# Kernel tuning notes

Hardware: AMD Instinct MI355X
Metric: run time of the kernel (lower is better)

Reference implementation:

```python
import jax, jax.numpy as jnp
import numpy as np

N_HEADS = 16
D_MODEL = 1024
D_K = D_MODEL // N_HEADS


def setup_inputs() -> dict:
    key = jax.random.key(0)
    ks = jax.random.split(key, 9)
    B, L = 4, 2048
    s = 1.0 / np.sqrt(D_MODEL)
    x = jax.random.normal(ks[0], (B, L, D_MODEL), dtype=jnp.float32)
    mask = jnp.tril(jnp.ones((L, L), dtype=jnp.int32))  # causal [L, L]
    Wq = jax.random.normal(ks[1], (D_MODEL, D_MODEL), dtype=jnp.float32) * s
    Wk = jax.random.normal(ks[2], (D_MODEL, D_MODEL), dtype=jnp.float32) * s
    Wv = jax.random.normal(ks[3], (D_MODEL, D_MODEL), dtype=jnp.float32) * s
    Wo = jax.random.normal(ks[4], (D_MODEL, D_MODEL), dtype=jnp.float32) * s
    bq = jnp.zeros((D_MODEL,), jnp.float32)
    bk = jnp.zeros((D_MODEL,), jnp.float32)
    bv = jnp.zeros((D_MODEL,), jnp.float32)
    bo = jnp.zeros((D_MODEL,), jnp.float32)
    return {"x": x, "mask": mask, "Wq": Wq, "bq": bq, "Wk": Wk, "bk": bk,
            "Wv": Wv, "bv": bv, "Wo": Wo, "bo": bo}


def reference(x, mask, Wq, bq, Wk, bk, Wv, bv, Wo, bo):
    B, L, _ = x.shape
    # projections -> [B, H, L, d_k]
    def split_heads(t):
        return t.reshape(B, L, N_HEADS, D_K).transpose(0, 2, 1, 3)
    Q = split_heads(x @ Wq + bq)
    K = split_heads(x @ Wk + bk)
    V = split_heads(x @ Wv + bv)
    orig_dtype = Q.dtype
    # fp32 upcast for scores (faithful to source)
    scores = jnp.einsum('bhqd,bhkd->bhqk', Q.astype(jnp.float32),
                        K.astype(jnp.float32)) / np.sqrt(D_K)
    # orig dtype is float32 -> masked fill with -inf
    scores = jnp.where(mask == 0, -jnp.inf, scores).astype(orig_dtype)
    attn = jax.nn.softmax(scores, axis=-1)  # dropout p=0 -> identity (eval)
    out = jnp.einsum('bhqk,bhkd->bhqd', attn, V)
    out = out.transpose(0, 2, 1, 3).reshape(B, L, D_MODEL)
    return out @ Wo + bo
```

## Files before the change

kernel.cpp:

```cpp
#include <hip/hip_runtime.h>

#define DMODEL 1024
#define NTOK   8192
#define SEQ    2048
#define NH     16
#define DK     64

typedef short short8  __attribute__((ext_vector_type(8)));
typedef short short4v __attribute__((ext_vector_type(4)));
typedef float floatx4 __attribute__((ext_vector_type(4)));

__device__ __forceinline__ unsigned short f2bf(float f) {
  unsigned int u = __float_as_uint(f);
  u += 0x7fffu + ((u >> 16) & 1u);
  return (unsigned short)(u >> 16);
}

__device__ __forceinline__ void async16(short* lds, const short* g) {
  __builtin_amdgcn_global_load_lds(
      (const __attribute__((address_space(1))) void*)g,
      (__attribute__((address_space(3))) void*)lds, 16, 0, 0);
}

__global__ void prep_kernel(const float* __restrict__ x, ushort4* __restrict__ xb,
                            const float* __restrict__ W0, const float* __restrict__ W1,
                            const float* __restrict__ W2, const float* __restrict__ W3,
                            short* __restrict__ T0, short* __restrict__ T1,
                            short* __restrict__ T2, short* __restrict__ T3) {
  const int z = blockIdx.z;
  const int tx = threadIdx.x, ty = threadIdx.y;
  if (z == 4) {
    const float4* xv = (const float4*)x;
    int i = (blockIdx.y * 32 + blockIdx.x) * 256 + ty * 32 + tx;
#pragma unroll
    for (int u = 0; u < 8; ++u) {
      int idx = i + u * 262144;
      float4 v = xv[idx];
      ushort4 o;
      o.x = f2bf(v.x); o.y = f2bf(v.y); o.z = f2bf(v.z); o.w = f2bf(v.w);
      xb[idx] = o;
    }
    return;
  }
  __shared__ float tile[32][33];
  const float* W = (z == 0) ? W0 : (z == 1) ? W1 : (z == 2) ? W2 : W3;
  short*      Wt = (z == 0) ? T0 : (z == 1) ? T1 : (z == 2) ? T2 : T3;
  int bx = blockIdx.x, by = blockIdx.y;
#pragma unroll
  for (int j = 0; j < 4; ++j)
    tile[ty + j * 8][tx] = W[(size_t)(by * 32 + ty + j * 8) * DMODEL + bx * 32 + tx];
  __syncthreads();
#pragma unroll
  for (int j = 0; j < 4; ++j)
    Wt[(size_t)(bx * 32 + ty + j * 8) * DMODEL + by * 32 + tx] =
        (short)f2bf(tile[tx][ty + j * 8]);
}

__global__ __launch_bounds__(256, 2) void gemm_qkv_fused(
    const short* __restrict__ xb,
    const short* __restrict__ Wqt, const short* __restrict__ Wkt, const short* __restrict__ Wvt,
    const float* __restrict__ bq,  const float* __restrict__ bk,  const float* __restrict__ bv,
    short* __restrict__ Qb, short* __restrict__ Kb, short* __restrict__ Vt) {
  __shared__ __align__(16) short As[128 * 64];
  __shared__ __align__(16) short Bs[3][128 * 64];
  const int tid = threadIdx.x, lane = tid & 63, w = tid >> 6;
  const int wm = w >> 1, wn = w & 1, ln = lane & 15, quad = lane >> 4;
  const int m0 = blockIdx.y * 128, n0 = blockIdx.x * 128;

  floatx4 acc[3][4][4];
#pragma unroll
  for (int z = 0; z < 3; ++z)
#pragma unroll
    for (int i = 0; i < 4; ++i)
#pragma unroll
      for (int j = 0; j < 4; ++j) acc[z][i][j] = (floatx4){0.f, 0.f, 0.f, 0.f};

  const int lr8 = lane >> 3, fch = ((lane & 7) ^ lr8) * 8;
  const short* ga  = xb  + (size_t)(m0 + lr8) * DMODEL + fch;
  const short* gb0 = Wqt + (size_t)(n0 + lr8) * DMODEL + fch;
  const short* gb1 = Wkt + (size_t)(n0 + lr8) * DMODEL + fch;
  const short* gb2 = Wvt + (size_t)(n0 + lr8) * DMODEL + fch;

  for (int kb = 0; kb < DMODEL; kb += 64) {
    __syncthreads();
#pragma unroll
    for (int i = 0; i < 4; ++i) {
      const int rb = w * 32 + i * 8;
      const size_t go = (size_t)rb * DMODEL + kb;
      async16(As + rb * 64,        ga  + go);
      async16((short*)Bs[0] + rb * 64, gb0 + go);
      async16((short*)Bs[1] + rb * 64, gb1 + go);
      async16((short*)Bs[2] + rb * 64, gb2 + go);
    }
    __syncthreads();
#pragma unroll
    for (int kk = 0; kk < 2; ++kk) {
      short8 af[4];
#pragma unroll
      for (int t = 0; t < 4; ++t) {
        int row = wm * 64 + t * 16 + ln;
        af[t] = *(const short8*)(As + row * 64 + ((kk * 4 + quad) ^ (row & 7)) * 8);
      }
#pragma unroll
      for (int z = 0; z < 3; ++z) {
        short8 bf[4];
#pragma unroll
        for (int t = 0; t < 4; ++t) {
          int row = wn * 64 + t * 16 + ln;
          bf[t] = *(const short8*)(Bs[z] + row * 64 + ((kk * 4 + quad) ^ (row & 7)) * 8);
        }
#pragma unroll
        for (int mt = 0; mt < 4; ++mt)
#pragma unroll
          for (int nt = 0; nt < 4; ++nt)
            acc[z][mt][nt] = __builtin_amdgcn_mfma_f32_16x16x32_bf16(af[mt], bf[nt], acc[z][mt][nt], 0, 0, 0);
      }
    }
  }

#pragma unroll
  for (int z = 0; z < 2; ++z) {
    const float* bias = z ? bk : bq;
    short* out        = z ? Kb : Qb;
    const float scale = z ? 1.0f : 0.18033688011112042f;
#pragma unroll
    for (int mt = 0; mt < 4; ++mt)
#pragma unroll
      for (int nt = 0; nt < 4; ++nt) {
        int n = n0 + wn * 64 + nt * 16 + ln;
        float bb = bias[n];
        int h = n >> 6, d = n & 63;
#pragma unroll
        for (int r = 0; r < 4; ++r) {
          int m = m0 + wm * 64 + mt * 16 + quad * 4 + r;
          int b = m >> 11, l = m & 2047;
          out[(size_t)(b * NH + h) * (SEQ * DK) + (size_t)l * DK + d] =
              (short)f2bf((acc[z][mt][nt][r] + bb) * scale);
        }
      }
  }
#pragma unroll
  for (int mt = 0; mt < 4; ++mt)
#pragma unroll
    for (int nt = 0; nt < 4; ++nt) {
      int n = n0 + wn * 64 + nt * 16 + ln;
      float bb = bv[n];
      int h = n >> 6, d = n & 63;
      int mb = m0 + wm * 64 + mt * 16 + quad * 4;
      int b = mb >> 11, l = mb & 2047;
      short4v pk;
#pragma unroll
      for (int r = 0; r < 4; ++r) pk[r] = (short)f2bf(acc[2][mt][nt][r] + bb);
      *(short4v*)(Vt + ((size_t)(b * NH + h) * DK + d) * SEQ + l) = pk;
    }
}

__global__ __launch_bounds__(256) void gemm_out(
    const short* __restrict__ Ob, const short* __restrict__ Wot,
    const float* __restrict__ bo, float* __restrict__ outp) {
  __shared__ __align__(16) short As[128 * 64];
  __shared__ __align__(16) short Bs[128 * 64];
  const int tid = threadIdx.x, lane = tid & 63, w = tid >> 6;
  const int wm = w >> 1, wn = w & 1, ln = lane & 15, quad = lane >> 4;
  const int m0 = blockIdx.y * 128, n0 = blockIdx.x * 128;
  floatx4 acc[4][4];
#pragma unroll
  for (int i = 0; i < 4; ++i)
#pragma unroll
    for (int j = 0; j < 4; ++j) acc[i][j] = (floatx4){0.f, 0.f, 0.f, 0.f};
  const int lr8 = lane >> 3, fch = ((lane & 7) ^ lr8) * 8;
  const short* ga = Ob  + (size_t)(m0 + lr8) * DMODEL + fch;
  const short* gb = Wot + (size_t)(n0 + lr8) * DMODEL + fch;
  for (int kb = 0; kb < DMODEL; kb += 64) {
    __syncthreads();
#pragma unroll
    for (int i = 0; i < 4; ++i) {
      const int rb = w * 32 + i * 8;
      const size_t go = (size_t)rb * DMODEL + kb;
      async16(As + rb * 64, ga + go);
      async16(Bs + rb * 64, gb + go);
    }
    __syncthreads();
#pragma unroll
    for (int kk = 0; kk < 2; ++kk) {
      short8 af[4], bf[4];
#pragma unroll
      for (int t = 0; t < 4; ++t) {
        int ra = wm * 64 + t * 16 + ln, rb2 = wn * 64 + t * 16 + ln;
        af[t] = *(const short8*)(As + ra * 64 + ((kk * 4 + quad) ^ (ra & 7)) * 8);
        bf[t] = *(const short8*)(Bs + rb2 * 64 + ((kk * 4 + quad) ^ (rb2 & 7)) * 8);
      }
#pragma unroll
      for (int mt = 0; mt < 4; ++mt)
#pragma unroll
        for (int nt = 0; nt < 4; ++nt)
          acc[mt][nt] = __builtin_amdgcn_mfma_f32_16x16x32_bf16(af[mt], bf[nt], acc[mt][nt], 0, 0, 0);
    }
  }
#pragma unroll
  for (int mt = 0; mt < 4; ++mt)
#pragma unroll
    for (int nt = 0; nt < 4; ++nt) {
      int n = n0 + wn * 64 + nt * 16 + ln;
      float bb = bo[n];
#pragma unroll
      for (int r = 0; r < 4; ++r) {
        int m = m0 + wm * 64 + mt * 16 + quad * 4 + r;
        outp[(size_t)m * DMODEL + n] = acc[mt][nt][r] + bb;
      }
    }
}

#define FMAX 12.0f

template <bool DOL>
__device__ __forceinline__ void attn_step(
    const short* __restrict__ Ks, const short* __restrict__ Vs,
    short* __restrict__ Ps0, short* __restrict__ Ps1,
    const short8 qfL[2], const short8 qfH[2],
    floatx4 accL[4], floatx4 accH[4], float& lstL, float& lstH,
    int qrowL, int qrowH, int kt, int qiL, int qiH,
    int ln, int quad, int w) {
  floatx4 sL[4], sH[4];
#pragma unroll
  for (int i = 0; i < 4; ++i) {
    if (DOL) sL[i] = (floatx4){0.f, 0.f, 0.f, 0.f};
    sH[i] = (floatx4){0.f, 0.f, 0.f, 0.f};
  }
#pragma unroll
  for (int kk = 0; kk < 2; ++kk)
#pragma unroll
    for (int t = 0; t < 4; ++t) {
      short8 kf = *(const short8*)(Ks + (t * 16 + ln) * 64 + ((kk * 4 + quad) ^ (ln & 7)) * 8);
      if (DOL) sL[t] = __builtin_amdgcn_mfma_f32_16x16x32_bf16(kf, qfL[kk], sL[t], 0, 0, 0);
      sH[t] = __builtin_amdgcn_mfma_f32_16x16x32_bf16(kf, qfH[kk], sH[t], 0, 0, 0);
    }
  if (DOL && kt == qiL) {
#pragma unroll
    for (int t = 0; t < 4; ++t)
#pragma unroll
      for (int r = 0; r < 4; ++r)
        if (kt * 64 + t * 16 + quad * 4 + r > qrowL) sL[t][r] = -1.0e30f;
  }
  if (kt == qiH) {
#pragma unroll
    for (int t = 0; t < 4; ++t)
#pragma unroll
      for (int r = 0; r < 4; ++r)
        if (kt * 64 + t * 16 + quad * 4 + r > qrowH) sH[t][r] = -1.0e30f;
  }
  if (DOL) {
    float rs = 0.f;
#pragma unroll
    for (int t = 0; t < 4; ++t) {
      float p0 = __builtin_amdgcn_exp2f(sL[t][0] - FMAX);
      float p1 = __builtin_amdgcn_exp2f(sL[t][1] - FMAX);
      float p2 = __builtin_amdgcn_exp2f(sL[t][2] - FMAX);
      float p3 = __builtin_amdgcn_exp2f(sL[t][3] - FMAX);
      rs += (p0 + p1) + (p2 + p3);
      uint2 pk;
      pk.x = __builtin_amdgcn_perm(__float_as_uint(p1), __float_as_uint(p0), 0x07060302u);
      pk.y = __builtin_amdgcn_perm(__float_as_uint(p3), __float_as_uint(p2), 0x07060302u);
      *(uint2*)(Ps0 + (w * 16 + ln) * 72 + t * 16 + quad * 4) = pk;
    }
    lstL += rs;
  }
  {
    float rs = 0.f;
#pragma unroll
    for (int t = 0; t < 4; ++t) {
      float p0 = __builtin_amdgcn_exp2f(sH[t][0] - FMAX);
      float p1 = __builtin_amdgcn_exp2f(sH[t][1] - FMAX);
      float p2 = __builtin_amdgcn_exp2f(sH[t][2] - FMAX);
      float p3 = __builtin_amdgcn_exp2f(sH[t][3] - FMAX);
      rs += (p0 + p1) + (p2 + p3);
      uint2 pk;
      pk.x = __builtin_amdgcn_perm(__float_as_uint(p1), __float_as_uint(p0), 0x07060302u);
      pk.y = __builtin_amdgcn_perm(__float_as_uint(p3), __float_as_uint(p2), 0x07060302u);
      *(uint2*)(Ps1 + (w * 16 + ln) * 72 + t * 16 + quad * 4) = pk;
    }
    lstH += rs;
  }
  __threadfence_block();
#pragma unroll
  for (int kk = 0; kk < 2; ++kk) {
    short8 pfL, pfH;
    if (DOL) pfL = *(const short8*)(Ps0 + (w * 16 + ln) * 72 + kk * 32 + quad * 8);
    pfH = *(const short8*)(Ps1 + (w * 16 + ln) * 72 + kk * 32 + quad * 8);
#pragma unroll
    for (int dt = 0; dt < 4; ++dt) {
      short8 vf = *(const short8*)(Vs + (dt * 16 + ln) * 64 + ((kk * 4 + quad) ^ (ln & 7)) * 8);
      if (DOL) accL[dt] = __builtin_amdgcn_mfma_f32_16x16x32_bf16(vf, pfL, accL[dt], 0, 0, 0);
      accH[dt] = __builtin_amdgcn_mfma_f32_16x16x32_bf16(vf, pfH, accH[dt], 0, 0, 0);
    }
  }
}

__global__ __launch_bounds__(256, 4) void attn_kernel(
    const short* __restrict__ Qb, const short* __restrict__ Kb,
    const short* __restrict__ Vt, short* __restrict__ Ob) {
  __shared__ __align__(16) short Ks[64 * 64];
  __shared__ __align__(16) short Vs[64 * 64];
  __shared__ __align__(16) short Ps[2][64 * 72];
  const int tid = threadIdx.x, lane = tid & 63, w = tid >> 6;
  const int ln = lane & 15, quad = lane >> 4;
  const int pr = blockIdx.x;
  const int bh = blockIdx.y;
  const int qiL = pr, qiH = 31 - pr;
  const short* Qh = Qb + (size_t)bh * (SEQ * DK);
  const short* Kh = Kb + (size_t)bh * (SEQ * DK);
  const short* Vh = Vt + (size_t)bh * (DK * SEQ);

  const int qrowL = qiL * 64 + w * 16 + ln;
  const int qrowH = qiH * 64 + w * 16 + ln;
  short8 qfL[2], qfH[2];
#pragma unroll
  for (int kk = 0; kk < 2; ++kk) {
    qfL[kk] = *(const short8*)(Qh + (size_t)qrowL * DK + kk * 32 + quad * 8);
    qfH[kk] = *(const short8*)(Qh + (size_t)qrowH * DK + kk * 32 + quad * 8);
  }

  floatx4 accL[4], accH[4];
#pragma unroll
  for (int i = 0; i < 4; ++i) {
    accL[i] = (floatx4){0.f, 0.f, 0.f, 0.f};
    accH[i] = (floatx4){0.f, 0.f, 0.f, 0.f};
  }
  float lstL = 0.f, lstH = 0.f;

  const int lr = lane >> 3, fch = (lane & 7) ^ lr;
  const int nktL = qiL + 1, nktH = qiH + 1;

  for (int kt = 0; kt < nktH; ++kt) {
    __syncthreads();
    const short* Kt = Kh + (size_t)kt * 64 * DK;
#pragma unroll
    for (int i = 0; i < 2; ++i) {
      int row = w * 16 + i * 8;
      async16(Ks + row * 64, Kt + (size_t)(row + lr) * DK + fch * 8);
      async16(Vs + row * 64, Vh + (size_t)(row + lr) * SEQ + kt * 64 + fch * 8);
    }
    __syncthreads();
    if (kt < nktL)
      attn_step<true>(Ks, Vs, Ps[0], Ps[1], qfL, qfH, accL, accH, lstL, lstH,
                      qrowL, qrowH, kt, qiL, qiH, ln, quad, w);
    else
      attn_step<false>(Ks, Vs, Ps[0], Ps[1], qfL, qfH, accL, accH, lstL, lstH,
                       qrowL, qrowH, kt, qiL, qiH, ln, quad, w);
  }

  const int b = bh >> 4, h = bh & 15;
#pragma unroll
  for (int g = 0; g < 2; ++g) {
    float l = g ? lstH : lstL;
    l += __shfl_xor(l, 16);
    l += __shfl_xor(l, 32);
    const floatx4* acc = g ? accH : accL;
    float inv = 1.0015f / l;
#pragma unroll
    for (int dt = 0; dt < 4; ++dt) {
      short4v o;
#pragma unroll
      for (int r = 0; r < 4; ++r) o[r] = (short)f2bf(acc[dt][r] * inv);
      *(short4v*)(Ps[g] + (w * 16 + ln) * 72 + dt * 16 + quad * 4) = o;
    }
  }
  __syncthreads();
  const int row = tid >> 2, c0 = (tid & 3) * 16;
#pragma unroll
  for (int g = 0; g < 2; ++g) {
    int qi = g ? qiH : qiL;
    short* dst = Ob + (size_t)(b * SEQ + qi * 64 + row) * DMODEL + h * DK + c0;
    const short* srcp = Ps[g] + row * 72 + c0;
    *(short8*)dst       = *(const short8*)srcp;
    *(short8*)(dst + 8) = *(const short8*)(srcp + 8);
  }
}

extern "C" void kernel_launch(void* const* d_in, const int* in_sizes, int n_in,
                              void* d_out, int out_size, void* d_ws, size_t ws_size,
                              hipStream_t stream) {
  (void)in_sizes; (void)n_in; (void)out_size; (void)ws_size;
  const float* x  = (const float*)d_in[0];
  const float* Wq = (const float*)d_in[2];
  const float* bq = (const float*)d_in[3];
  const float* Wk = (const float*)d_in[4];
  const float* bk = (const float*)d_in[5];
  const float* Wv = (const float*)d_in[6];
  const float* bv = (const float*)d_in[7];
  const float* Wo = (const float*)d_in[8];
  const float* bo = (const float*)d_in[9];

  char* ws = (char*)d_ws;
  short* xb  = (short*)(ws);
  short* Wqt = (short*)(ws + ((size_t)16 << 20));
  short* Wkt = (short*)(ws + ((size_t)18 << 20));
  short* Wvt = (short*)(ws + ((size_t)20 << 20));
  short* Wot = (short*)(ws + ((size_t)22 << 20));
  short* Qb  = (short*)(ws + ((size_t)24 << 20));
  short* Kb  = (short*)(ws + ((size_t)40 << 20));
  short* Vtg = (short*)(ws + ((size_t)56 << 20));
  short* Ob  = (short*)(ws + ((size_t)72 << 20));

  prep_kernel<<<dim3(32, 32, 5), dim3(32, 8), 0, stream>>>(
      x, (ushort4*)xb, Wq, Wk, Wv, Wo, Wqt, Wkt, Wvt, Wot);

  gemm_qkv_fused<<<dim3(DMODEL / 128, NTOK / 128), 256, 0, stream>>>(
      xb, Wqt, Wkt, Wvt, bq, bk, bv, Qb, Kb, Vtg);

  attn_kernel<<<dim3(16, 4 * NH), 256, 0, stream>>>(Qb, Kb, Vtg, Ob);

  gemm_out<<<dim3(DMODEL / 128, NTOK / 128), 256, 0, stream>>>(Ob, Wot, bo, (float*)d_out);
}
```

Measured before the change: 265.6 us.

## Register-prefetch K/V tiles, compute row sums via MFMA, swizzle attention block order

The attention kernel now prefetches the next K/V tile into registers while the current tile is computed, replacing the global-to-LDS async loads. The softmax row sum is accumulated with an MFMA against a vector of bf16 ones, which removes the scalar adds and cross-lane shuffles, and the -FMAX offset is folded into the score accumulator's initial value. The grid becomes 1D with a swizzled block-to-(head, pair) mapping to spread work across XCDs. The denominator now sums the bf16-rounded probabilities, consistent with the PV product, and the 1.0015 fudge factor is dropped. In exchange the prefetch costs extra registers and two MFMAs per step.

Result: slower. 465.6 us (+75.3%).

```diff
diff --git a/kernel.cpp b/kernel.cpp
--- a/kernel.cpp
+++ b/kernel.cpp
@@ -217,15 +217,15 @@
 __device__ __forceinline__ void attn_step(
     const short* __restrict__ Ks, const short* __restrict__ Vs,
     short* __restrict__ Ps0, short* __restrict__ Ps1,
-    const short8 qfL[2], const short8 qfH[2],
-    floatx4 accL[4], floatx4 accH[4], float& lstL, float& lstH,
+    const short8 qfL[2], const short8 qfH[2], const short8 ones,
+    floatx4 accL[4], floatx4 accH[4], floatx4& accSL, floatx4& accSH,
     int qrowL, int qrowH, int kt, int qiL, int qiH,
     int ln, int quad, int w) {
   floatx4 sL[4], sH[4];
 #pragma unroll
   for (int i = 0; i < 4; ++i) {
-    if (DOL) sL[i] = (floatx4){0.f, 0.f, 0.f, 0.f};
-    sH[i] = (floatx4){0.f, 0.f, 0.f, 0.f};
+    if (DOL) sL[i] = (floatx4){-FMAX, -FMAX, -FMAX, -FMAX};
+    sH[i] = (floatx4){-FMAX, -FMAX, -FMAX, -FMAX};
   }
 #pragma unroll
   for (int kk = 0; kk < 2; ++kk)
@@ -250,36 +250,30 @@
         if (kt * 64 + t * 16 + quad * 4 + r > qrowH) sH[t][r] = -1.0e30f;
   }
   if (DOL) {
-    float rs = 0.f;
 #pragma unroll
     for (int t = 0; t < 4; ++t) {
-      float p0 = __builtin_amdgcn_exp2f(sL[t][0] - FMAX);
-      float p1 = __builtin_amdgcn_exp2f(sL[t][1] - FMAX);
-      float p2 = __builtin_amdgcn_exp2f(sL[t][2] - FMAX);
-      float p3 = __builtin_amdgcn_exp2f(sL[t][3] - FMAX);
-      rs += (p0 + p1) + (p2 + p3);
+      float p0 = __builtin_amdgcn_exp2f(sL[t][0]);
+      float p1 = __builtin_amdgcn_exp2f(sL[t][1]);
+      float p2 = __builtin_amdgcn_exp2f(sL[t][2]);
+      float p3 = __builtin_amdgcn_exp2f(sL[t][3]);
       uint2 pk;
       pk.x = __builtin_amdgcn_perm(__float_as_uint(p1), __float_as_uint(p0), 0x07060302u);
       pk.y = __builtin_amdgcn_perm(__float_as_uint(p3), __float_as_uint(p2), 0x07060302u);
       *(uint2*)(Ps0 + (w * 16 + ln) * 72 + t * 16 + quad * 4) = pk;
     }
-    lstL += rs;
   }
   {
-    float rs = 0.f;
 #pragma unroll
     for (int t = 0; t < 4; ++t) {
-      float p0 = __builtin_amdgcn_exp2f(sH[t][0] - FMAX);
-      float p1 = __builtin_amdgcn_exp2f(sH[t][1] - FMAX);
-      float p2 = __builtin_amdgcn_exp2f(sH[t][2] - FMAX);
-      float p3 = __builtin_amdgcn_exp2f(sH[t][3] - FMAX);
-      rs += (p0 + p1) + (p2 + p3);
+      float p0 = __builtin_amdgcn_exp2f(sH[t][0]);
+      float p1 = __builtin_amdgcn_exp2f(sH[t][1]);
+      float p2 = __builtin_amdgcn_exp2f(sH[t][2]);
+      float p3 = __builtin_amdgcn_exp2f(sH[t][3]);
       uint2 pk;
       pk.x = __builtin_amdgcn_perm(__float_as_uint(p1), __float_as_uint(p0), 0x07060302u);
       pk.y = __builtin_amdgcn_perm(__float_as_uint(p3), __float_as_uint(p2), 0x07060302u);
       *(uint2*)(Ps1 + (w * 16 + ln) * 72 + t * 16 + quad * 4) = pk;
     }
-    lstH += rs;
   }
   __threadfence_block();
 #pragma unroll
@@ -287,6 +281,8 @@
     short8 pfL, pfH;
     if (DOL) pfL = *(const short8*)(Ps0 + (w * 16 + ln) * 72 + kk * 32 + quad * 8);
     pfH = *(const short8*)(Ps1 + (w * 16 + ln) * 72 + kk * 32 + quad * 8);
+    if (DOL) accSL = __builtin_amdgcn_mfma_f32_16x16x32_bf16(ones, pfL, accSL, 0, 0, 0);
+    accSH = __builtin_amdgcn_mfma_f32_16x16x32_bf16(ones, pfH, accSH, 0, 0, 0);
 #pragma unroll
     for (int dt = 0; dt < 4; ++dt) {
       short8 vf = *(const short8*)(Vs + (dt * 16 + ln) * 64 + ((kk * 4 + quad) ^ (ln & 7)) * 8);
@@ -304,8 +300,10 @@
   __shared__ __align__(16) short Ps[2][64 * 72];
   const int tid = threadIdx.x, lane = tid & 63, w = tid >> 6;
   const int ln = lane & 15, quad = lane >> 4;
-  const int pr = blockIdx.x;
-  const int bh = blockIdx.y;
+  const int lin = blockIdx.x;
+  const int v   = (lin & 7) * 128 + (lin >> 3);
+  const int bh  = v >> 4;
+  const int pr  = v & 15;
   const int qiL = pr, qiH = 31 - pr;
   const short* Qh = Qb + (size_t)bh * (SEQ * DK);
   const short* Kh = Kb + (size_t)bh * (SEQ * DK);
@@ -319,44 +317,80 @@
     qfL[kk] = *(const short8*)(Qh + (size_t)qrowL * DK + kk * 32 + quad * 8);
     qfH[kk] = *(const short8*)(Qh + (size_t)qrowH * DK + kk * 32 + quad * 8);
   }
-
-  floatx4 accL[4], accH[4];
+  short8 ones;
+#pragma unroll
+  for (int j = 0; j < 8; ++j) ones[j] = (short)0x3F80;
+
+  floatx4 accL[4], accH[4], accSL, accSH;
 #pragma unroll
   for (int i = 0; i < 4; ++i) {
     accL[i] = (floatx4){0.f, 0.f, 0.f, 0.f};
     accH[i] = (floatx4){0.f, 0.f, 0.f, 0.f};
   }
-  float lstL = 0.f, lstH = 0.f;
+  accSL = (floatx4){0.f, 0.f, 0.f, 0.f};
+  accSH = (floatx4){0.f, 0.f, 0.f, 0.f};
 
   const int lr = lane >> 3, fch = (lane & 7) ^ lr;
   const int nktL = qiL + 1, nktH = qiH + 1;
 
+  uint4 rkA[2], rvA[2], rkB[2], rvB[2];
+#pragma unroll
+  for (int i = 0; i < 2; ++i) {
+    int row = w * 16 + i * 8;
+    rkA[i] = *(const uint4*)(Kh + (size_t)(row + lr) * DK + fch * 8);
+    rvA[i] = *(const uint4*)(Vh + (size_t)(row + lr) * SEQ + fch * 8);
+  }
+
   for (int kt = 0; kt < nktH; ++kt) {
     __syncthreads();
-    const short* Kt = Kh + (size_t)kt * 64 * DK;
-#pragma unroll
-    for (int i = 0; i < 2; ++i) {
-      int row = w * 16 + i * 8;
-      async16(Ks + row * 64, Kt + (size_t)(row + lr) * DK + fch * 8);
-      async16(Vs + row * 64, Vh + (size_t)(row + lr) * SEQ + kt * 64 + fch * 8);
-    }
-    __syncthreads();
+    if ((kt & 1) == 0) {
+#pragma unroll
+      for (int i = 0; i < 2; ++i) {
+        int row = w * 16 + i * 8;
+        *(uint4*)(Ks + row * 64 + lane * 8) = rkA[i];
+        *(uint4*)(Vs + row * 64 + lane * 8) = rvA[i];
+      }
+    } else {
+#pragma unroll
+      for (int i = 0; i < 2; ++i) {
+        int row = w * 16 + i * 8;
+        *(uint4*)(Ks + row * 64 + lane * 8) = rkB[i];
+        *(uint4*)(Vs + row * 64 + lane * 8) = rvB[i];
+      }
+    }
+    __syncthreads();
+    if (kt + 1 < nktH) {
+      const short* Kt = Kh + (size_t)(kt + 1) * 64 * DK;
+      if ((kt & 1) == 0) {
+#pragma unroll
+        for (int i = 0; i < 2; ++i) {
+          int row = w * 16 + i * 8;
+          rkB[i] = *(const uint4*)(Kt + (size_t)(row + lr) * DK + fch * 8);
+          rvB[i] = *(const uint4*)(Vh + (size_t)(row + lr) * SEQ + (kt + 1) * 64 + fch * 8);
+        }
+      } else {
+#pragma unroll
+        for (int i = 0; i < 2; ++i) {
+          int row = w * 16 + i * 8;
+          rkA[i] = *(const uint4*)(Kt + (size_t)(row + lr) * DK + fch * 8);
+          rvA[i] = *(const uint4*)(Vh + (size_t)(row + lr) * SEQ + (kt + 1) * 64 + fch * 8);
+        }
+      }
+    }
     if (kt < nktL)
-      attn_step<true>(Ks, Vs, Ps[0], Ps[1], qfL, qfH, accL, accH, lstL, lstH,
+      attn_step<true>(Ks, Vs, Ps[0], Ps[1], qfL, qfH, ones, accL, accH, accSL, accSH,
                       qrowL, qrowH, kt, qiL, qiH, ln, quad, w);
     else
-      attn_step<false>(Ks, Vs, Ps[0], Ps[1], qfL, qfH, accL, accH, lstL, lstH,
+      attn_step<false>(Ks, Vs, Ps[0], Ps[1], qfL, qfH, ones, accL, accH, accSL, accSH,
                        qrowL, qrowH, kt, qiL, qiH, ln, quad, w);
   }
 
   const int b = bh >> 4, h = bh & 15;
 #pragma unroll
   for (int g = 0; g < 2; ++g) {
-    float l = g ? lstH : lstL;
-    l += __shfl_xor(l, 16);
-    l += __shfl_xor(l, 32);
+    float l = g ? accSH[0] : accSL[0];
     const floatx4* acc = g ? accH : accL;
-    float inv = 1.0015f / l;
+    float inv = 1.0f / l;
 #pragma unroll
     for (int dt = 0; dt < 4; ++dt) {
       short4v o;
@@ -408,7 +442,7 @@
   gemm_qkv_fused<<<dim3(DMODEL / 128, NTOK / 128), 256, 0, stream>>>(
       xb, Wqt, Wkt, Wvt, bq, bk, bv, Qb, Kb, Vtg);
 
-  attn_kernel<<<dim3(16, 4 * NH), 256, 0, stream>>>(Qb, Kb, Vtg, Ob);
+  attn_kernel<<<dim3(16 * 4 * NH), 256, 0, stream>>>(Qb, Kb, Vtg, Ob);
 
   gemm_out<<<dim3(DMODEL / 128, NTOK / 128), 256, 0, stream>>>(Ob, Wot, bo, (float*)d_out);
 }
```
